# Kernel optimization log

Hardware: AMD Instinct MI355X
Metric: run time of the kernel (lower is better)

The kernel has to match this reference:

```python
import jax, jax.numpy as jnp
import numpy as np

BS, SLEN, DIM, N_HEADS = 2, 2048, 2048, 16
DH = DIM // N_HEADS


def setup_inputs() -> dict:
    key = jax.random.key(0)
    ks = jax.random.split(key, 10)
    s = DIM ** -0.5
    x = jax.random.normal(ks[0], (BS, SLEN, DIM), dtype=jnp.float32)
    # causal attention mask from get_masks: True = attend
    mask = jnp.tril(jnp.ones((SLEN, SLEN), dtype=bool))[None].repeat(BS, axis=0)
    Wq = jax.random.normal(ks[1], (DIM, DIM), jnp.float32) * s
    bq = jnp.zeros((DIM,), jnp.float32)
    Wk = jax.random.normal(ks[2], (DIM, DIM), jnp.float32) * s
    bk = jnp.zeros((DIM,), jnp.float32)
    Wv = jax.random.normal(ks[3], (DIM, DIM), jnp.float32) * s
    bv = jnp.zeros((DIM,), jnp.float32)
    Wo = jax.random.normal(ks[4], (DIM, DIM), jnp.float32) * s
    bo = jnp.zeros((DIM,), jnp.float32)
    # normalized_attention learned scalar, init 1/sqrt(dim_per_head)
    scale = jnp.asarray(1.0 / np.sqrt(DH), dtype=jnp.float32)
    return {"x": x, "mask": mask, "Wq": Wq, "bq": bq, "Wk": Wk, "bk": bk,
            "Wv": Wv, "bv": bv, "Wo": Wo, "bo": bo, "scale": scale}


def _split_heads(t):  # (bs, slen, dim) -> (bs, H, slen, dh)
    return t.reshape(BS, -1, N_HEADS, DH).transpose(0, 2, 1, 3)


def reference(x, mask, Wq, bq, Wk, bk, Wv, bv, Wo, bo, scale):
    # QKV projections (torch Linear: x @ W.T + b)
    q = _split_heads(x @ Wq.T + bq)
    k = _split_heads(x @ Wk.T + bk)
    v = _split_heads(x @ Wv.T + bv)
    # normalized attention: L2-normalize q, k on head dim, learned scalar scale
    q = q / jnp.linalg.norm(q, axis=-1, keepdims=True)
    k = k / jnp.linalg.norm(k, axis=-1, keepdims=True)
    q = q * scale
    scores = jnp.einsum('bhqd,bhkd->bhqk', q, k)  # (bs, H, qlen, klen)
    scores = jnp.where(mask[:, None, :, :], scores, -jnp.inf)
    weights = jax.nn.softmax(scores, axis=-1)  # dropout p=0 / eval
    ctx = jnp.einsum('bhqk,bhkd->bhqd', weights, v)
    ctx = ctx.transpose(0, 2, 1, 3).reshape(BS, SLEN, DIM)
    return ctx @ Wo.T + bo
```

## Files before the change

kernel.cpp:

```cpp
#include <hip/hip_runtime.h>
#include <hip/hip_bf16.h>

#define S_LEN 2048
#define DIMN  2048
#define NHEAD 16
#define DHEAD 128
#define SEGQ  ((size_t)4096 * 2048)
#define SEGW  ((size_t)2048 * 2048)

typedef __attribute__((ext_vector_type(8))) short short8;
typedef __attribute__((ext_vector_type(4))) float floatx4;

__device__ inline float bf2f(unsigned short u) {
    union { unsigned int i; float f; } v; v.i = ((unsigned int)u) << 16; return v.f;
}
__device__ inline unsigned short f2bf(float f) {
    unsigned int x = __float_as_uint(f);
    unsigned int r = (x + 0x7FFFu + ((x >> 16) & 1u)) >> 16;
    return (unsigned short)r;
}
__device__ inline short8 ld8_f32_as_bf16(const float* p) {
    float4 a = *(const float4*)p;
    float4 b = *(const float4*)(p + 4);
    short8 r;
    r[0] = (short)f2bf(a.x); r[1] = (short)f2bf(a.y);
    r[2] = (short)f2bf(a.z); r[3] = (short)f2bf(a.w);
    r[4] = (short)f2bf(b.x); r[5] = (short)f2bf(b.y);
    r[6] = (short)f2bf(b.z); r[7] = (short)f2bf(b.w);
    return r;
}
__device__ inline void glds16(unsigned short* lds, const unsigned short* g) {
    __builtin_amdgcn_global_load_lds(
        (const __attribute__((address_space(1))) unsigned int*)g,
        (__attribute__((address_space(3))) unsigned int*)lds, 16, 0, 0);
}

#define SBAR() do { __builtin_amdgcn_sched_barrier(0); \
                    __builtin_amdgcn_s_barrier();      \
                    __builtin_amdgcn_sched_barrier(0); } while (0)

__global__ __launch_bounds__(256) void cvt5_kernel(
    const float* __restrict__ s0, const float* __restrict__ s1,
    const float* __restrict__ s2, const float* __restrict__ s3,
    const float* __restrict__ s4,
    unsigned short* __restrict__ d0, unsigned short* __restrict__ d1,
    unsigned short* __restrict__ d2, unsigned short* __restrict__ d3,
    unsigned short* __restrict__ d4)
{
    const float* s; unsigned short* d; size_t n;
    switch (blockIdx.y) {
        case 0:  s = s0; d = d0; n = SEGQ; break;
        case 1:  s = s1; d = d1; n = SEGW; break;
        case 2:  s = s2; d = d2; n = SEGW; break;
        case 3:  s = s3; d = d3; n = SEGW; break;
        default: s = s4; d = d4; n = SEGW; break;
    }
    size_t stride = (size_t)gridDim.x * 256 * 8;
    for (size_t i = ((size_t)blockIdx.x * 256 + threadIdx.x) * 8; i < n; i += stride)
        *(short8*)&d[i] = ld8_f32_as_bf16(&s[i]);
}

#define BUFE (384 * 32)

template <int EPI>
__global__ __launch_bounds__(512) void gemm3(
    const unsigned short* __restrict__ A, const unsigned short* __restrict__ Bw,
    const float* __restrict__ b0, const float* __restrict__ b1,
    const float* __restrict__ b2, const float* __restrict__ scale_p,
    void* __restrict__ Cp, int M, int N, int K)
{
    __shared__ __align__(16) unsigned short sBuf[3 * BUFE];

    const int tid  = threadIdx.x;
    const int w    = tid >> 6, lane = tid & 63;
    const int l15  = lane & 15, quad = lane >> 4;
    const int wr   = w >> 1, wc = w & 1;
    const int tm   = blockIdx.y * 256, tn = blockIdx.x * 128;

    const int colE = ((lane & 3) * 8) ^ (((lane >> 3) & 3) << 3);
    const int cs   = (quad * 8) ^ (((l15 >> 1) & 3) << 3);
    const int srow = w * 16 + (lane >> 2);

    floatx4 acc[4][4] = {};

    auto stage = [&](int kt, int bsel) {
        const int k0 = kt * 32;
        glds16(&sBuf[bsel * BUFE + 0 * 4096 + w * 512],
               &A[(size_t)(tm + srow) * K + k0 + colE]);
        glds16(&sBuf[bsel * BUFE + 1 * 4096 + w * 512],
               &A[(size_t)(tm + 128 + srow) * K + k0 + colE]);
        glds16(&sBuf[bsel * BUFE + 8192 + w * 512],
               &Bw[(size_t)(tn + srow) * K + k0 + colE]);
    };

    const int nT = K >> 5;
    stage(0, 0);
    stage(1, 1);

    int bs = 0;
    for (int t = 0; t < nT; ++t) {
        if (t < nT - 1) asm volatile("s_waitcnt vmcnt(3)" ::: "memory");
        else            asm volatile("s_waitcnt vmcnt(0)" ::: "memory");
        __builtin_amdgcn_s_barrier();
        __builtin_amdgcn_sched_barrier(0);

        const unsigned short* bufA = &sBuf[bs * BUFE];
        const unsigned short* bufB = bufA + 8192;
        short8 af[4], bfr[4];
#pragma unroll
        for (int mi = 0; mi < 4; mi++)
            af[mi] = *(const short8*)&bufA[(wr * 64 + mi * 16 + l15) * 32 + cs];
#pragma unroll
        for (int ni = 0; ni < 4; ni++)
            bfr[ni] = *(const short8*)&bufB[(wc * 64 + ni * 16 + l15) * 32 + cs];

        if (t + 2 < nT) stage(t + 2, bs == 0 ? 2 : bs - 1);

        __builtin_amdgcn_s_setprio(1);
#pragma unroll
        for (int mi = 0; mi < 4; mi++)
#pragma unroll
            for (int ni = 0; ni < 4; ni++)
                acc[mi][ni] = __builtin_amdgcn_mfma_f32_16x16x32_bf16(af[mi], bfr[ni], acc[mi][ni], 0, 0, 0);
        __builtin_amdgcn_s_setprio(0);

        bs = (bs == 2) ? 0 : bs + 1;
    }
    __syncthreads();

    if (EPI == 0) {
        const int t = tn >> 11;
        const float* bp = (t == 0) ? b0 : (t == 1) ? b1 : b2;
        unsigned short* Q = (unsigned short*)Cp;
#pragma unroll
        for (int ni = 0; ni < 4; ni++) {
            int n = tn + wc * 64 + ni * 16 + l15;
            float bias = bp[n & 2047];
#pragma unroll
            for (int mi = 0; mi < 4; mi++)
#pragma unroll
                for (int r = 0; r < 4; r++) acc[mi][ni][r] += bias;
        }
        float ssq[4][4];
#pragma unroll
        for (int mi = 0; mi < 4; mi++)
#pragma unroll
            for (int r = 0; r < 4; r++) {
                float s = 0.0f;
#pragma unroll
                for (int ni = 0; ni < 4; ni++) s += acc[mi][ni][r] * acc[mi][ni][r];
#pragma unroll
                for (int off = 1; off < 16; off <<= 1) s += __shfl_xor(s, off, 64);
                ssq[mi][r] = s;
            }
        float* ssh = (float*)sBuf;
        if (l15 == 0) {
#pragma unroll
            for (int mi = 0; mi < 4; mi++)
#pragma unroll
                for (int r = 0; r < 4; r++)
                    ssh[wc * 256 + wr * 64 + mi * 16 + quad * 4 + r] = ssq[mi][r];
        }
        __syncthreads();
        const float scl = (t == 0) ? scale_p[0] : 1.0f;
#pragma unroll
        for (int mi = 0; mi < 4; mi++) {
            int mbase = tm + wr * 64 + mi * 16 + quad * 4;
#pragma unroll
            for (int r = 0; r < 4; r++) {
                float tot = ssq[mi][r] + ssh[(wc ^ 1) * 256 + wr * 64 + mi * 16 + quad * 4 + r];
                float f = (t < 2) ? rsqrtf(tot) * scl : 1.0f;
                int m = mbase + r;
                int b = m >> 11, s = m & 2047;
#pragma unroll
                for (int ni = 0; ni < 4; ni++) {
                    int n = tn + wc * 64 + ni * 16 + l15;
                    int h = (n >> 7) & 15, dh = n & 127;
                    float v = acc[mi][ni][r] * f;
                    size_t idx = (t < 2)
                        ? (size_t)t * SEGQ + (((size_t)(b * NHEAD + h)) * S_LEN + s) * DHEAD + dh
                        : 2 * SEGQ + (((size_t)(b * NHEAD + h)) * DHEAD + dh) * S_LEN + s;
                    Q[idx] = f2bf(v);
                }
            }
        }
    } else {
#pragma unroll
        for (int mi = 0; mi < 4; mi++) {
            int mbase = tm + wr * 64 + mi * 16 + quad * 4;
#pragma unroll
            for (int ni = 0; ni < 4; ni++) {
                int n = tn + wc * 64 + ni * 16 + l15;
                float bias = b0[n];
#pragma unroll
                for (int r = 0; r < 4; r++) {
                    int m = mbase + r;
                    ((float*)Cp)[(size_t)m * N + n] = acc[mi][ni][r] + bias;
                }
            }
        }
    }
}

template <int SPLIT, int A_F32, int OUT_F32>
__global__ __launch_bounds__(256) void gemm_bt(
    const void* __restrict__ Ap, const float* __restrict__ Bw,
    const float* __restrict__ bias, void* __restrict__ Cp,
    int M, int N, int K)
{
    __shared__ __align__(16) unsigned short sA[128 * 40];
    __shared__ __align__(16) unsigned short sB[128 * 40];

    const int tid  = threadIdx.x;
    const int w    = tid >> 6, lane = tid & 63;
    const int l15  = lane & 15, quad = lane >> 4;
    const int wm   = w >> 1, wn = w & 1;
    const int tm   = blockIdx.y * 128, tn = blockIdx.x * 128;

    const float*          Af32 = (const float*)Ap;
    const unsigned short* Abf  = (const unsigned short*)Ap;

    floatx4 acc[4][4] = {};

    for (int k0 = 0; k0 < K; k0 += 32) {
        __syncthreads();
#pragma unroll
        for (int i = 0; i < 2; i++) {
            int c   = tid + i * 256;
            int row = c >> 2;
            int kc  = (c & 3) * 8;
            size_t goff = (size_t)(tm + row) * K + k0 + kc;
            if (A_F32)
                *(short8*)&sA[row * 40 + kc] = ld8_f32_as_bf16(&Af32[goff]);
            else
                *(short8*)&sA[row * 40 + kc] = *(const short8*)&Abf[goff];
            *(short8*)&sB[row * 40 + kc] =
                ld8_f32_as_bf16(&Bw[(size_t)(tn + row) * K + k0 + kc]);
        }
        __syncthreads();

        short8 af[4], bfr[4];
#pragma unroll
        for (int mi = 0; mi < 4; mi++)
            af[mi] = *(const short8*)&sA[(wm * 64 + mi * 16 + l15) * 40 + quad * 8];
#pragma unroll
        for (int ni = 0; ni < 4; ni++)
            bfr[ni] = *(const short8*)&sB[(wn * 64 + ni * 16 + l15) * 40 + quad * 8];
#pragma unroll
        for (int mi = 0; mi < 4; mi++)
#pragma unroll
            for (int ni = 0; ni < 4; ni++)
                acc[mi][ni] = __builtin_amdgcn_mfma_f32_16x16x32_bf16(af[mi], bfr[ni], acc[mi][ni], 0, 0, 0);
    }

#pragma unroll
    for (int mi = 0; mi < 4; mi++) {
        int mbase = tm + wm * 64 + mi * 16 + quad * 4;
#pragma unroll
        for (int ni = 0; ni < 4; ni++) {
            int n = tn + wn * 64 + ni * 16 + l15;
            float bv = bias[n];
#pragma unroll
            for (int r = 0; r < 4; r++) {
                int m = mbase + r;
                float v = acc[mi][ni][r] + bv;
                if (SPLIT == 1) {
                    int b = m >> 11, s = m & 2047, h = n >> 7, dh = n & 127;
                    ((unsigned short*)Cp)[(((size_t)(b * NHEAD + h)) * S_LEN + s) * DHEAD + dh] = f2bf(v);
                } else if (SPLIT == 2) {
                    int b = m >> 11, s = m & 2047, h = n >> 7, dh = n & 127;
                    ((unsigned short*)Cp)[(((size_t)(b * NHEAD + h)) * DHEAD + dh) * S_LEN + s] = f2bf(v);
                } else if (OUT_F32) {
                    ((float*)Cp)[(size_t)m * N + n] = v;
                } else {
                    ((unsigned short*)Cp)[(size_t)m * N + n] = f2bf(v);
                }
            }
        }
    }
}

__global__ __launch_bounds__(256) void l2norm_kernel(
    unsigned short* __restrict__ qn, unsigned short* __restrict__ kn,
    const float* __restrict__ scale_p)
{
    const int w = threadIdx.x >> 6, lane = threadIdx.x & 63;
    size_t row = (size_t)blockIdx.x * 4 + w;
    unsigned short* base = (blockIdx.y == 0 ? qn : kn) + row * DHEAD;
    float a = bf2f(base[lane * 2]);
    float b = bf2f(base[lane * 2 + 1]);
    float ss = a * a + b * b;
#pragma unroll
    for (int off = 1; off < 64; off <<= 1) ss += __shfl_xor(ss, off, 64);
    float f = rsqrtf(ss);
    if (blockIdx.y == 0) f *= scale_p[0];
    base[lane * 2]     = f2bf(a * f);
    base[lane * 2 + 1] = f2bf(b * f);
}

__global__ __launch_bounds__(512) void attn_kernel6(
    const unsigned short* __restrict__ qn, const unsigned short* __restrict__ kn,
    const unsigned short* __restrict__ vt, unsigned short* __restrict__ ctx)
{
    __shared__ __align__(16) unsigned short sK [128 * 128];
    __shared__ __align__(16) unsigned short sVt[128 * 128];
    __shared__ __align__(16) unsigned short sP [8 * 16 * 128];

    const int tid  = threadIdx.x;
    const int w    = tid >> 6, lane = tid & 63;
    const int l15  = lane & 15, quad = lane >> 4;
    const int lin  = blockIdx.x + (blockIdx.y << 3);
    const int xb   = (lin >> 3) & 7;
    const int bh   = ((lin & 7) << 2) | (lin >> 6);
    const size_t headoff = (size_t)bh * S_LEN * DHEAD;
    const unsigned short* kbase0 = kn + headoff;
    const unsigned short* vtbase = vt + headoff;
    unsigned short* sPw = sP + w * 16 * 128;

    short8 kpre[4], vpre[4];

    for (int half = 0; half < 2; half++) {
        const int qt = half ? (15 - xb) : xb;

        const unsigned short* qrow = qn + headoff + (size_t)(qt * 128 + w * 16 + l15) * DHEAD;
        short8 aQ[4];
#pragma unroll
        for (int ks = 0; ks < 4; ks++) aQ[ks] = *(const short8*)(qrow + ks * 32 + quad * 8);

        floatx4 O[8] = {};
        float m_i[4], l_i[4];
#pragma unroll
        for (int r = 0; r < 4; r++) { m_i[r] = -1e30f; l_i[r] = 0.0f; }

        if (half == 0) {
#pragma unroll
            for (int j = 0; j < 4; j++) {
                int c = tid + j * 512;
                kpre[j] = *(const short8*)(kbase0 + (size_t)(c >> 4) * DHEAD + (c & 15) * 8);
                vpre[j] = *(const short8*)(vtbase + (size_t)(c >> 4) * S_LEN + (c & 15) * 8);
            }
        }

        for (int kt = 0; kt <= qt; kt++) {
            SBAR();

#pragma unroll
            for (int j = 0; j < 4; j++) {
                int c = tid + j * 512;
                int row = c >> 4;
                int sl  = (c & 15) ^ (row & 15);
                *(short8*)&sK [row * 128 + sl * 8] = kpre[j];
                *(short8*)&sVt[row * 128 + sl * 8] = vpre[j];
            }

            if (kt < qt || half == 0) {
                const int knext = (kt < qt) ? (kt + 1) * 128 : 0;
#pragma unroll
                for (int j = 0; j < 4; j++) {
                    int c = tid + j * 512;
                    kpre[j] = *(const short8*)(kbase0 + (size_t)(knext + (c >> 4)) * DHEAD + (c & 15) * 8);
                    vpre[j] = *(const short8*)(vtbase + (size_t)(c >> 4) * S_LEN + knext + (c & 15) * 8);
                }
            }
            asm volatile("s_waitcnt lgkmcnt(0)" ::: "memory");
            SBAR();

            floatx4 sc[8] = {};
            __builtin_amdgcn_s_setprio(1);
#pragma unroll
            for (int ks = 0; ks < 4; ks++) {
#pragma unroll
                for (int ni = 0; ni < 8; ni++) {
                    short8 bK = *(const short8*)&sK[(ni * 16 + l15) * 128 + (((ks * 4 + quad) ^ l15) * 8)];
                    sc[ni] = __builtin_amdgcn_mfma_f32_16x16x32_bf16(aQ[ks], bK, sc[ni], 0, 0, 0);
                }
            }
            __builtin_amdgcn_s_setprio(0);

            if (kt == qt) {
#pragma unroll
                for (int ni = 0; ni < 8; ni++) {
                    int cl = ni * 16 + l15;
#pragma unroll
                    for (int r = 0; r < 4; r++) {
                        int rl = w * 16 + quad * 4 + r;
                        if (cl > rl) sc[ni][r] = -1e30f;
                    }
                }
            }

            float rmax[4];
#pragma unroll
            for (int r = 0; r < 4; r++) {
                float mx = sc[0][r];
#pragma unroll
                for (int ni = 1; ni < 8; ni++) mx = fmaxf(mx, sc[ni][r]);
                rmax[r] = mx;
            }
#pragma unroll
            for (int off = 1; off < 16; off <<= 1)
#pragma unroll
                for (int r = 0; r < 4; r++) rmax[r] = fmaxf(rmax[r], __shfl_xor(rmax[r], off, 64));

            float alpha[4], rsum[4];
#pragma unroll
            for (int r = 0; r < 4; r++) {
                float mn = fmaxf(m_i[r], rmax[r]);
                alpha[r] = exp2f((m_i[r] - mn) * 1.44269504f);
                m_i[r] = mn;
                rsum[r] = 0.0f;
            }
#pragma unroll
            for (int ni = 0; ni < 8; ni++) {
#pragma unroll
                for (int r = 0; r < 4; r++) {
                    float p = exp2f((sc[ni][r] - m_i[r]) * 1.44269504f);
                    rsum[r] += p;
                    int prow = quad * 4 + r;
                    sPw[prow * 128 + ((ni * 16 + l15) ^ ((prow & 15) << 3))] = f2bf(p);
                }
            }
#pragma unroll
            for (int off = 1; off < 16; off <<= 1)
#pragma unroll
                for (int r = 0; r < 4; r++) rsum[r] += __shfl_xor(rsum[r], off, 64);
#pragma unroll
            for (int r = 0; r < 4; r++) l_i[r] = l_i[r] * alpha[r] + rsum[r];
#pragma unroll
            for (int t = 0; t < 8; t++)
#pragma unroll
                for (int r = 0; r < 4; r++) O[t][r] *= alpha[r];


            __builtin_amdgcn_s_setprio(1);
#pragma unroll
            for (int ks2 = 0; ks2 < 4; ks2++) {
                short8 aP = *(const short8*)&sPw[l15 * 128 + ((ks2 * 32 + quad * 8) ^ (l15 << 3))];
#pragma unroll
                for (int t = 0; t < 8; t++) {
                    short8 bV = *(const short8*)&sVt[(t * 16 + l15) * 128 + (((ks2 * 4 + quad) ^ l15) * 8)];
                    O[t] = __builtin_amdgcn_mfma_f32_16x16x32_bf16(aP, bV, O[t], 0, 0, 0);
                }
            }
            __builtin_amdgcn_s_setprio(0);
        }

        const int b = bh >> 4, h = bh & 15;
#pragma unroll
        for (int r = 0; r < 4; r++) {
            float inv = 1.0f / l_i[r];
            int srow = qt * 128 + w * 16 + quad * 4 + r;
            size_t rowoff = ((size_t)(b * S_LEN + srow)) * DIMN + h * DHEAD;
#pragma unroll
            for (int t = 0; t < 8; t++)
                ctx[rowoff + t * 16 + l15] = f2bf(O[t][r] * inv);
        }
    }
}

extern "C" void kernel_launch(void* const* d_in, const int* in_sizes, int n_in,
                              void* d_out, int out_size, void* d_ws, size_t ws_size,
                              hipStream_t stream)
{
    const float* x     = (const float*)d_in[0];
    const float* Wq    = (const float*)d_in[2];
    const float* bq    = (const float*)d_in[3];
    const float* Wk    = (const float*)d_in[4];
    const float* bk    = (const float*)d_in[5];
    const float* Wv    = (const float*)d_in[6];
    const float* bv    = (const float*)d_in[7];
    const float* Wo    = (const float*)d_in[8];
    const float* bo    = (const float*)d_in[9];
    const float* scale = (const float*)d_in[10];

    const int M = 4096, N = 2048, K = 2048;
    float* out = (float*)d_out;
    const size_t need = (SEGQ + 4 * SEGW + 3 * SEGQ) * sizeof(unsigned short);

    if (ws_size >= need) {
        unsigned short* xb  = (unsigned short*)d_ws;
        unsigned short* wqb = xb  + SEGQ;
        unsigned short* wkb = wqb + SEGW;
        unsigned short* wvb = wkb + SEGW;
        unsigned short* wob = wvb + SEGW;
        unsigned short* qn  = wob + SEGW;
        unsigned short* kn  = qn  + SEGQ;
        unsigned short* vtb = kn  + SEGQ;
        unsigned short* ctx = xb;

        cvt5_kernel<<<dim3(512, 5), 256, 0, stream>>>(x, Wq, Wk, Wv, Wo,
                                                      xb, wqb, wkb, wvb, wob);
        gemm3<0><<<dim3(48, 16), 512, 0, stream>>>(xb, wqb, bq, bk, bv, scale, qn, M, 6144, K);
        attn_kernel6<<<dim3(8, 32), 512, 0, stream>>>(qn, kn, vtb, ctx);
        gemm3<1><<<dim3(16, 16), 512, 0, stream>>>(ctx, wob, bo, nullptr, nullptr, nullptr, out, M, N, K);
    } else {
        unsigned short* qn  = (unsigned short*)d_ws;
        unsigned short* kn  = qn + SEGQ;
        unsigned short* vtb = kn + SEGQ;
        unsigned short* ctx = vtb + SEGQ;

        gemm_bt<1, 1, 0><<<dim3(16, 32), 256, 0, stream>>>(x, Wq, bq, qn, M, N, K);
        gemm_bt<1, 1, 0><<<dim3(16, 32), 256, 0, stream>>>(x, Wk, bk, kn, M, N, K);
        gemm_bt<2, 1, 0><<<dim3(16, 32), 256, 0, stream>>>(x, Wv, bv, vtb, M, N, K);
        l2norm_kernel<<<dim3(16384, 2), 256, 0, stream>>>(qn, kn, scale);
        attn_kernel6<<<dim3(8, 32), 512, 0, stream>>>(qn, kn, vtb, ctx);
        gemm_bt<0, 0, 1><<<dim3(16, 32), 256, 0, stream>>>(ctx, Wo, bo, out, M, N, K);
    }
}
```

Baseline: 408.9 us.

## Halve attention key tile to 64 and switch GEMM to double buffering

The attention kernel now processes key/value tiles of 64 instead of 128, halving its shared memory. It also doubles the number of key iterations, masks by absolute position on the diagonal tiles, and adds a launch-bounds occupancy hint. The GEMM drops from a three-buffer LDS pipeline with two tiles in flight to a two-buffer scheme that issues the next stage after a full vmcnt(0) wait. This reduces LDS use, but the GEMM now has less load/compute overlap, and attention runs more barrier-synchronised iterations with smaller MFMA batches.

```diff
diff --git a/kernel.cpp b/kernel.cpp
--- a/kernel.cpp
+++ b/kernel.cpp
@@ -69,7 +69,7 @@
     const float* __restrict__ b2, const float* __restrict__ scale_p,
     void* __restrict__ Cp, int M, int N, int K)
 {
-    __shared__ __align__(16) unsigned short sBuf[3 * BUFE];
+    __shared__ __align__(16) unsigned short sBuf[2 * BUFE];
 
     const int tid  = threadIdx.x;
     const int w    = tid >> 6, lane = tid & 63;
@@ -95,16 +95,16 @@
 
     const int nT = K >> 5;
     stage(0, 0);
-    stage(1, 1);
-
-    int bs = 0;
+
+    int cur = 0;
     for (int t = 0; t < nT; ++t) {
-        if (t < nT - 1) asm volatile("s_waitcnt vmcnt(3)" ::: "memory");
-        else            asm volatile("s_waitcnt vmcnt(0)" ::: "memory");
+        asm volatile("s_waitcnt vmcnt(0)" ::: "memory");
         __builtin_amdgcn_s_barrier();
         __builtin_amdgcn_sched_barrier(0);
 
-        const unsigned short* bufA = &sBuf[bs * BUFE];
+        if (t + 1 < nT) stage(t + 1, cur ^ 1);
+
+        const unsigned short* bufA = &sBuf[cur * BUFE];
         const unsigned short* bufB = bufA + 8192;
         short8 af[4], bfr[4];
 #pragma unroll
@@ -113,8 +113,6 @@
 #pragma unroll
         for (int ni = 0; ni < 4; ni++)
             bfr[ni] = *(const short8*)&bufB[(wc * 64 + ni * 16 + l15) * 32 + cs];
-
-        if (t + 2 < nT) stage(t + 2, bs == 0 ? 2 : bs - 1);
 
         __builtin_amdgcn_s_setprio(1);
 #pragma unroll
@@ -124,7 +122,7 @@
                 acc[mi][ni] = __builtin_amdgcn_mfma_f32_16x16x32_bf16(af[mi], bfr[ni], acc[mi][ni], 0, 0, 0);
         __builtin_amdgcn_s_setprio(0);
 
-        bs = (bs == 2) ? 0 : bs + 1;
+        cur ^= 1;
     }
     __syncthreads();
 
@@ -298,13 +296,13 @@
     base[lane * 2 + 1] = f2bf(b * f);
 }
 
-__global__ __launch_bounds__(512) void attn_kernel6(
+__global__ __launch_bounds__(512, 4) void attn_kernel7(
     const unsigned short* __restrict__ qn, const unsigned short* __restrict__ kn,
     const unsigned short* __restrict__ vt, unsigned short* __restrict__ ctx)
 {
-    __shared__ __align__(16) unsigned short sK [128 * 128];
-    __shared__ __align__(16) unsigned short sVt[128 * 128];
-    __shared__ __align__(16) unsigned short sP [8 * 16 * 128];
+    __shared__ __align__(16) unsigned short sK [64 * 128];
+    __shared__ __align__(16) unsigned short sVt[128 * 64];
+    __shared__ __align__(16) unsigned short sP [8 * 16 * 64];
 
     const int tid  = threadIdx.x;
     const int w    = tid >> 6, lane = tid & 63;
@@ -315,12 +313,13 @@
     const size_t headoff = (size_t)bh * S_LEN * DHEAD;
     const unsigned short* kbase0 = kn + headoff;
     const unsigned short* vtbase = vt + headoff;
-    unsigned short* sPw = sP + w * 16 * 128;
-
-    short8 kpre[4], vpre[4];
+    unsigned short* sPw = sP + w * 16 * 64;
+
+    short8 kpre[2], vpre[2];
 
     for (int half = 0; half < 2; half++) {
-        const int qt = half ? (15 - xb) : xb;
+        const int qt  = half ? (15 - xb) : xb;
+        const int nkt = 2 * qt + 2;
 
         const unsigned short* qrow = qn + headoff + (size_t)(qt * 128 + w * 16 + l15) * DHEAD;
         short8 aQ[4];
@@ -334,56 +333,58 @@
 
         if (half == 0) {
 #pragma unroll
-            for (int j = 0; j < 4; j++) {
+            for (int j = 0; j < 2; j++) {
                 int c = tid + j * 512;
                 kpre[j] = *(const short8*)(kbase0 + (size_t)(c >> 4) * DHEAD + (c & 15) * 8);
-                vpre[j] = *(const short8*)(vtbase + (size_t)(c >> 4) * S_LEN + (c & 15) * 8);
-            }
-        }
-
-        for (int kt = 0; kt <= qt; kt++) {
+                vpre[j] = *(const short8*)(vtbase + (size_t)(c >> 3) * S_LEN + (c & 7) * 8);
+            }
+        }
+
+        for (int kt = 0; kt < nkt; kt++) {
             SBAR();
 
 #pragma unroll
-            for (int j = 0; j < 4; j++) {
-                int c = tid + j * 512;
-                int row = c >> 4;
-                int sl  = (c & 15) ^ (row & 15);
-                *(short8*)&sK [row * 128 + sl * 8] = kpre[j];
-                *(short8*)&sVt[row * 128 + sl * 8] = vpre[j];
-            }
-
-            if (kt < qt || half == 0) {
-                const int knext = (kt < qt) ? (kt + 1) * 128 : 0;
-#pragma unroll
-                for (int j = 0; j < 4; j++) {
+            for (int j = 0; j < 2; j++) {
+                int c  = tid + j * 512;
+                int kr = c >> 4;
+                int ks_ = (c & 15) ^ (kr & 15);
+                *(short8*)&sK[kr * 128 + ks_ * 8] = kpre[j];
+                int vr = c >> 3;
+                int vs = (c & 7) ^ (vr & 7);
+                *(short8*)&sVt[vr * 64 + vs * 8] = vpre[j];
+            }
+
+            if (kt + 1 < nkt || half == 0) {
+                const int knext = (kt + 1 < nkt) ? (kt + 1) * 64 : 0;
+#pragma unroll
+                for (int j = 0; j < 2; j++) {
                     int c = tid + j * 512;
                     kpre[j] = *(const short8*)(kbase0 + (size_t)(knext + (c >> 4)) * DHEAD + (c & 15) * 8);
-                    vpre[j] = *(const short8*)(vtbase + (size_t)(c >> 4) * S_LEN + knext + (c & 15) * 8);
+                    vpre[j] = *(const short8*)(vtbase + (size_t)(c >> 3) * S_LEN + knext + (c & 7) * 8);
                 }
             }
             asm volatile("s_waitcnt lgkmcnt(0)" ::: "memory");
             SBAR();
 
-            floatx4 sc[8] = {};
+            floatx4 sc[4] = {};
             __builtin_amdgcn_s_setprio(1);
 #pragma unroll
             for (int ks = 0; ks < 4; ks++) {
 #pragma unroll
-                for (int ni = 0; ni < 8; ni++) {
+                for (int ni = 0; ni < 4; ni++) {
                     short8 bK = *(const short8*)&sK[(ni * 16 + l15) * 128 + (((ks * 4 + quad) ^ l15) * 8)];
                     sc[ni] = __builtin_amdgcn_mfma_f32_16x16x32_bf16(aQ[ks], bK, sc[ni], 0, 0, 0);
                 }
             }
             __builtin_amdgcn_s_setprio(0);
 
-            if (kt == qt) {
-#pragma unroll
-                for (int ni = 0; ni < 8; ni++) {
-                    int cl = ni * 16 + l15;
+            if ((kt >> 1) == qt) {
+#pragma unroll
+                for (int ni = 0; ni < 4; ni++) {
+                    int cl = kt * 64 + ni * 16 + l15;
 #pragma unroll
                     for (int r = 0; r < 4; r++) {
-                        int rl = w * 16 + quad * 4 + r;
+                        int rl = qt * 128 + w * 16 + quad * 4 + r;
                         if (cl > rl) sc[ni][r] = -1e30f;
                     }
                 }
@@ -394,7 +395,7 @@
             for (int r = 0; r < 4; r++) {
                 float mx = sc[0][r];
 #pragma unroll
-                for (int ni = 1; ni < 8; ni++) mx = fmaxf(mx, sc[ni][r]);
+                for (int ni = 1; ni < 4; ni++) mx = fmaxf(mx, sc[ni][r]);
                 rmax[r] = mx;
             }
 #pragma unroll
@@ -411,13 +412,14 @@
                 rsum[r] = 0.0f;
             }
 #pragma unroll
-            for (int ni = 0; ni < 8; ni++) {
+            for (int ni = 0; ni < 4; ni++) {
 #pragma unroll
                 for (int r = 0; r < 4; r++) {
                     float p = exp2f((sc[ni][r] - m_i[r]) * 1.44269504f);
                     rsum[r] += p;
                     int prow = quad * 4 + r;
-                    sPw[prow * 128 + ((ni * 16 + l15) ^ ((prow & 15) << 3))] = f2bf(p);
+                    int slot = (ni * 2 + (l15 >> 3)) ^ (prow & 7);
+                    sPw[prow * 64 + slot * 8 + (l15 & 7)] = f2bf(p);
                 }
             }
 #pragma unroll
@@ -434,11 +436,11 @@
 
             __builtin_amdgcn_s_setprio(1);
 #pragma unroll
-            for (int ks2 = 0; ks2 < 4; ks2++) {
-                short8 aP = *(const short8*)&sPw[l15 * 128 + ((ks2 * 32 + quad * 8) ^ (l15 << 3))];
+            for (int ks2 = 0; ks2 < 2; ks2++) {
+                short8 aP = *(const short8*)&sPw[l15 * 64 + (((ks2 * 4 + quad) ^ (l15 & 7)) * 8)];
 #pragma unroll
                 for (int t = 0; t < 8; t++) {
-                    short8 bV = *(const short8*)&sVt[(t * 16 + l15) * 128 + (((ks2 * 4 + quad) ^ l15) * 8)];
+                    short8 bV = *(const short8*)&sVt[(t * 16 + l15) * 64 + (((ks2 * 4 + quad) ^ (l15 & 7)) * 8)];
                     O[t] = __builtin_amdgcn_mfma_f32_16x16x32_bf16(aP, bV, O[t], 0, 0, 0);
                 }
             }
@@ -491,7 +493,7 @@
         cvt5_kernel<<<dim3(512, 5), 256, 0, stream>>>(x, Wq, Wk, Wv, Wo,
                                                       xb, wqb, wkb, wvb, wob);
         gemm3<0><<<dim3(48, 16), 512, 0, stream>>>(xb, wqb, bq, bk, bv, scale, qn, M, 6144, K);
-        attn_kernel6<<<dim3(8, 32), 512, 0, stream>>>(qn, kn, vtb, ctx);
+        attn_kernel7<<<dim3(8, 32), 512, 0, stream>>>(qn, kn, vtb, ctx);
         gemm3<1><<<dim3(16, 16), 512, 0, stream>>>(ctx, wob, bo, nullptr, nullptr, nullptr, out, M, N, K);
     } else {
         unsigned short* qn  = (unsigned short*)d_ws;
@@ -503,7 +505,7 @@
         gemm_bt<1, 1, 0><<<dim3(16, 32), 256, 0, stream>>>(x, Wk, bk, kn, M, N, K);
         gemm_bt<2, 1, 0><<<dim3(16, 32), 256, 0, stream>>>(x, Wv, bv, vtb, M, N, K);
         l2norm_kernel<<<dim3(16384, 2), 256, 0, stream>>>(qn, kn, scale);
-        attn_kernel6<<<dim3(8, 32), 512, 0, stream>>>(qn, kn, vtb, ctx);
+        attn_kernel7<<<dim3(8, 32), 512, 0, stream>>>(qn, kn, vtb, ctx);
         gemm_bt<0, 0, 1><<<dim3(16, 32), 256, 0, stream>>>(ctx, Wo, bo, out, M, N, K);
     }
 }
```

Measured after the change: 547.7 us. +34.0%, slower.

## Split attention into one q-tile per block, chunk P buffer to cut LDS

Applied to the files above, without the earlier changes.

Replaces paired light/heavy q-tile processing with 512 blocks each handling one q-tile, ordered heaviest-first. The P staging buffer is halved by doing softmax-exponent and P·V in two 64-key chunks, and launch bounds request higher occupancy. The aim is to fit more blocks per CU and hide latency better. It risks register spills under the tighter bound and less predictable load balance than the explicit pairing.

```diff
diff --git a/kernel.cpp b/kernel.cpp
--- a/kernel.cpp
+++ b/kernel.cpp
@@ -298,144 +298,136 @@
     base[lane * 2 + 1] = f2bf(b * f);
 }
 
-__global__ __launch_bounds__(512) void attn_kernel6(
+__global__ __launch_bounds__(512, 4) void attn_kernel8(
     const unsigned short* __restrict__ qn, const unsigned short* __restrict__ kn,
     const unsigned short* __restrict__ vt, unsigned short* __restrict__ ctx)
 {
     __shared__ __align__(16) unsigned short sK [128 * 128];
     __shared__ __align__(16) unsigned short sVt[128 * 128];
-    __shared__ __align__(16) unsigned short sP [8 * 16 * 128];
+    __shared__ __align__(16) unsigned short sP [8 * 16 * 64];
 
     const int tid  = threadIdx.x;
     const int w    = tid >> 6, lane = tid & 63;
     const int l15  = lane & 15, quad = lane >> 4;
-    const int lin  = blockIdx.x + (blockIdx.y << 3);
-    const int xb   = (lin >> 3) & 7;
-    const int bh   = ((lin & 7) << 2) | (lin >> 6);
+    const int lin  = blockIdx.x;
+    const int qt   = 15 - (lin >> 5);
+    const int bh   = lin & 31;
     const size_t headoff = (size_t)bh * S_LEN * DHEAD;
     const unsigned short* kbase0 = kn + headoff;
     const unsigned short* vtbase = vt + headoff;
-    unsigned short* sPw = sP + w * 16 * 128;
+    unsigned short* sPw = sP + w * 16 * 64;
 
     short8 kpre[4], vpre[4];
 
-    for (int half = 0; half < 2; half++) {
-        const int qt = half ? (15 - xb) : xb;
-
-        const unsigned short* qrow = qn + headoff + (size_t)(qt * 128 + w * 16 + l15) * DHEAD;
-        short8 aQ[4];
-#pragma unroll
-        for (int ks = 0; ks < 4; ks++) aQ[ks] = *(const short8*)(qrow + ks * 32 + quad * 8);
-
-        floatx4 O[8] = {};
-        float m_i[4], l_i[4];
-#pragma unroll
-        for (int r = 0; r < 4; r++) { m_i[r] = -1e30f; l_i[r] = 0.0f; }
-
-        if (half == 0) {
+    const unsigned short* qrow = qn + headoff + (size_t)(qt * 128 + w * 16 + l15) * DHEAD;
+    short8 aQ[4];
+#pragma unroll
+    for (int ks = 0; ks < 4; ks++) aQ[ks] = *(const short8*)(qrow + ks * 32 + quad * 8);
+
+    floatx4 O[8] = {};
+    float m_i[4], l_i[4];
+#pragma unroll
+    for (int r = 0; r < 4; r++) { m_i[r] = -1e30f; l_i[r] = 0.0f; }
+
+#pragma unroll
+    for (int j = 0; j < 4; j++) {
+        int c = tid + j * 512;
+        kpre[j] = *(const short8*)(kbase0 + (size_t)(c >> 4) * DHEAD + (c & 15) * 8);
+        vpre[j] = *(const short8*)(vtbase + (size_t)(c >> 4) * S_LEN + (c & 15) * 8);
+    }
+
+    for (int kt = 0; kt <= qt; kt++) {
+        SBAR();
+
+#pragma unroll
+        for (int j = 0; j < 4; j++) {
+            int c = tid + j * 512;
+            int row = c >> 4;
+            int sl  = (c & 15) ^ (row & 15);
+            *(short8*)&sK [row * 128 + sl * 8] = kpre[j];
+            *(short8*)&sVt[row * 128 + sl * 8] = vpre[j];
+        }
+
+        if (kt < qt) {
+            const int knext = (kt + 1) * 128;
 #pragma unroll
             for (int j = 0; j < 4; j++) {
                 int c = tid + j * 512;
-                kpre[j] = *(const short8*)(kbase0 + (size_t)(c >> 4) * DHEAD + (c & 15) * 8);
-                vpre[j] = *(const short8*)(vtbase + (size_t)(c >> 4) * S_LEN + (c & 15) * 8);
-            }
-        }
-
-        for (int kt = 0; kt <= qt; kt++) {
-            SBAR();
-
-#pragma unroll
-            for (int j = 0; j < 4; j++) {
-                int c = tid + j * 512;
-                int row = c >> 4;
-                int sl  = (c & 15) ^ (row & 15);
-                *(short8*)&sK [row * 128 + sl * 8] = kpre[j];
-                *(short8*)&sVt[row * 128 + sl * 8] = vpre[j];
-            }
-
-            if (kt < qt || half == 0) {
-                const int knext = (kt < qt) ? (kt + 1) * 128 : 0;
-#pragma unroll
-                for (int j = 0; j < 4; j++) {
-                    int c = tid + j * 512;
-                    kpre[j] = *(const short8*)(kbase0 + (size_t)(knext + (c >> 4)) * DHEAD + (c & 15) * 8);
-                    vpre[j] = *(const short8*)(vtbase + (size_t)(c >> 4) * S_LEN + knext + (c & 15) * 8);
+                kpre[j] = *(const short8*)(kbase0 + (size_t)(knext + (c >> 4)) * DHEAD + (c & 15) * 8);
+                vpre[j] = *(const short8*)(vtbase + (size_t)(c >> 4) * S_LEN + knext + (c & 15) * 8);
+            }
+        }
+        asm volatile("s_waitcnt lgkmcnt(0)" ::: "memory");
+        SBAR();
+
+        floatx4 sc[8] = {};
+        __builtin_amdgcn_s_setprio(1);
+#pragma unroll
+        for (int ks = 0; ks < 4; ks++) {
+#pragma unroll
+            for (int ni = 0; ni < 8; ni++) {
+                short8 bK = *(const short8*)&sK[(ni * 16 + l15) * 128 + (((ks * 4 + quad) ^ l15) * 8)];
+                sc[ni] = __builtin_amdgcn_mfma_f32_16x16x32_bf16(aQ[ks], bK, sc[ni], 0, 0, 0);
+            }
+        }
+        __builtin_amdgcn_s_setprio(0);
+
+        if (kt == qt) {
+#pragma unroll
+            for (int ni = 0; ni < 8; ni++) {
+                int cl = ni * 16 + l15;
+#pragma unroll
+                for (int r = 0; r < 4; r++) {
+                    int rl = w * 16 + quad * 4 + r;
+                    if (cl > rl) sc[ni][r] = -1e30f;
                 }
             }
-            asm volatile("s_waitcnt lgkmcnt(0)" ::: "memory");
-            SBAR();
-
-            floatx4 sc[8] = {};
-            __builtin_amdgcn_s_setprio(1);
-#pragma unroll
-            for (int ks = 0; ks < 4; ks++) {
-#pragma unroll
-                for (int ni = 0; ni < 8; ni++) {
-                    short8 bK = *(const short8*)&sK[(ni * 16 + l15) * 128 + (((ks * 4 + quad) ^ l15) * 8)];
-                    sc[ni] = __builtin_amdgcn_mfma_f32_16x16x32_bf16(aQ[ks], bK, sc[ni], 0, 0, 0);
-                }
-            }
-            __builtin_amdgcn_s_setprio(0);
-
-            if (kt == qt) {
-#pragma unroll
-                for (int ni = 0; ni < 8; ni++) {
-                    int cl = ni * 16 + l15;
-#pragma unroll
-                    for (int r = 0; r < 4; r++) {
-                        int rl = w * 16 + quad * 4 + r;
-                        if (cl > rl) sc[ni][r] = -1e30f;
-                    }
-                }
-            }
-
-            float rmax[4];
-#pragma unroll
-            for (int r = 0; r < 4; r++) {
-                float mx = sc[0][r];
-#pragma unroll
-                for (int ni = 1; ni < 8; ni++) mx = fmaxf(mx, sc[ni][r]);
-                rmax[r] = mx;
-            }
-#pragma unroll
-            for (int off = 1; off < 16; off <<= 1)
-#pragma unroll
-                for (int r = 0; r < 4; r++) rmax[r] = fmaxf(rmax[r], __shfl_xor(rmax[r], off, 64));
-
-            float alpha[4], rsum[4];
-#pragma unroll
-            for (int r = 0; r < 4; r++) {
-                float mn = fmaxf(m_i[r], rmax[r]);
-                alpha[r] = exp2f((m_i[r] - mn) * 1.44269504f);
-                m_i[r] = mn;
-                rsum[r] = 0.0f;
-            }
-#pragma unroll
-            for (int ni = 0; ni < 8; ni++) {
+        }
+
+        float rmax[4];
+#pragma unroll
+        for (int r = 0; r < 4; r++) {
+            float mx = sc[0][r];
+#pragma unroll
+            for (int ni = 1; ni < 8; ni++) mx = fmaxf(mx, sc[ni][r]);
+            rmax[r] = mx;
+        }
+#pragma unroll
+        for (int off = 1; off < 16; off <<= 1)
+#pragma unroll
+            for (int r = 0; r < 4; r++) rmax[r] = fmaxf(rmax[r], __shfl_xor(rmax[r], off, 64));
+
+        float alpha[4], rsum[4];
+#pragma unroll
+        for (int r = 0; r < 4; r++) {
+            float mn = fmaxf(m_i[r], rmax[r]);
+            alpha[r] = exp2f((m_i[r] - mn) * 1.44269504f);
+            m_i[r] = mn;
+            rsum[r] = 0.0f;
+        }
+#pragma unroll
+        for (int t = 0; t < 8; t++)
+#pragma unroll
+            for (int r = 0; r < 4; r++) O[t][r] *= alpha[r];
+
+#pragma unroll
+        for (int chunk = 0; chunk < 2; chunk++) {
+#pragma unroll
+            for (int ni4 = 0; ni4 < 4; ni4++) {
+                int ni = chunk * 4 + ni4;
 #pragma unroll
                 for (int r = 0; r < 4; r++) {
                     float p = exp2f((sc[ni][r] - m_i[r]) * 1.44269504f);
                     rsum[r] += p;
                     int prow = quad * 4 + r;
-                    sPw[prow * 128 + ((ni * 16 + l15) ^ ((prow & 15) << 3))] = f2bf(p);
+                    sPw[prow * 64 + (((ni4 * 2 + (l15 >> 3)) ^ (prow & 7)) * 8) + (l15 & 7)] = f2bf(p);
                 }
             }
-#pragma unroll
-            for (int off = 1; off < 16; off <<= 1)
-#pragma unroll
-                for (int r = 0; r < 4; r++) rsum[r] += __shfl_xor(rsum[r], off, 64);
-#pragma unroll
-            for (int r = 0; r < 4; r++) l_i[r] = l_i[r] * alpha[r] + rsum[r];
-#pragma unroll
-            for (int t = 0; t < 8; t++)
-#pragma unroll
-                for (int r = 0; r < 4; r++) O[t][r] *= alpha[r];
-
-
             __builtin_amdgcn_s_setprio(1);
 #pragma unroll
-            for (int ks2 = 0; ks2 < 4; ks2++) {
-                short8 aP = *(const short8*)&sPw[l15 * 128 + ((ks2 * 32 + quad * 8) ^ (l15 << 3))];
+            for (int k2 = 0; k2 < 2; k2++) {
+                int ks2 = chunk * 2 + k2;
+                short8 aP = *(const short8*)&sPw[l15 * 64 + (((k2 * 4 + quad) ^ (l15 & 7)) * 8)];
 #pragma unroll
                 for (int t = 0; t < 8; t++) {
                     short8 bV = *(const short8*)&sVt[(t * 16 + l15) * 128 + (((ks2 * 4 + quad) ^ l15) * 8)];
@@ -444,17 +436,23 @@
             }
             __builtin_amdgcn_s_setprio(0);
         }
-
-        const int b = bh >> 4, h = bh & 15;
-#pragma unroll
-        for (int r = 0; r < 4; r++) {
-            float inv = 1.0f / l_i[r];
-            int srow = qt * 128 + w * 16 + quad * 4 + r;
-            size_t rowoff = ((size_t)(b * S_LEN + srow)) * DIMN + h * DHEAD;
-#pragma unroll
-            for (int t = 0; t < 8; t++)
-                ctx[rowoff + t * 16 + l15] = f2bf(O[t][r] * inv);
-        }
+#pragma unroll
+        for (int off = 1; off < 16; off <<= 1)
+#pragma unroll
+            for (int r = 0; r < 4; r++) rsum[r] += __shfl_xor(rsum[r], off, 64);
+#pragma unroll
+        for (int r = 0; r < 4; r++) l_i[r] = l_i[r] * alpha[r] + rsum[r];
+    }
+
+    const int b = bh >> 4, h = bh & 15;
+#pragma unroll
+    for (int r = 0; r < 4; r++) {
+        float inv = 1.0f / l_i[r];
+        int srow = qt * 128 + w * 16 + quad * 4 + r;
+        size_t rowoff = ((size_t)(b * S_LEN + srow)) * DIMN + h * DHEAD;
+#pragma unroll
+        for (int t = 0; t < 8; t++)
+            ctx[rowoff + t * 16 + l15] = f2bf(O[t][r] * inv);
     }
 }
 
@@ -491,7 +489,7 @@
         cvt5_kernel<<<dim3(512, 5), 256, 0, stream>>>(x, Wq, Wk, Wv, Wo,
                                                       xb, wqb, wkb, wvb, wob);
         gemm3<0><<<dim3(48, 16), 512, 0, stream>>>(xb, wqb, bq, bk, bv, scale, qn, M, 6144, K);
-        attn_kernel6<<<dim3(8, 32), 512, 0, stream>>>(qn, kn, vtb, ctx);
+        attn_kernel8<<<dim3(512), 512, 0, stream>>>(qn, kn, vtb, ctx);
         gemm3<1><<<dim3(16, 16), 512, 0, stream>>>(ctx, wob, bo, nullptr, nullptr, nullptr, out, M, N, K);
     } else {
         unsigned short* qn  = (unsigned short*)d_ws;
@@ -503,7 +501,7 @@
         gemm_bt<1, 1, 0><<<dim3(16, 32), 256, 0, stream>>>(x, Wk, bk, kn, M, N, K);
         gemm_bt<2, 1, 0><<<dim3(16, 32), 256, 0, stream>>>(x, Wv, bv, vtb, M, N, K);
         l2norm_kernel<<<dim3(16384, 2), 256, 0, stream>>>(qn, kn, scale);
-        attn_kernel6<<<dim3(8, 32), 512, 0, stream>>>(qn, kn, vtb, ctx);
+        attn_kernel8<<<dim3(512), 512, 0, stream>>>(qn, kn, vtb, ctx);
         gemm_bt<0, 0, 1><<<dim3(16, 32), 256, 0, stream>>>(ctx, Wo, bo, out, M, N, K);
     }
 }
```

Result: slower. 553.1 us (+35.3%).
